# Kernel optimization log

Hardware: AMD Instinct MI355X
Metric: run time of the kernel (lower is better)

Reference implementation:

```python
import jax, jax.numpy as jnp
import numpy as np

# __init__ constants
COORS_RANGE = ((-51.2, 51.2), (-51.2, 51.2), (-4.0, 2.4))  # x, y, z ranges
SPATIAL = (512, 512, 64)  # base spatial shape (X, Y, Z)
SCALES = (2, 4, 8, 1)     # scale_list + [1]
N_POINTS = 2_000_000
N_BATCH = 8


def setup_inputs() -> dict:
    key = jax.random.key(0)
    kp, kb = jax.random.split(key)
    lo = jnp.array([r[0] for r in COORS_RANGE], dtype=jnp.float32)
    hi = jnp.array([r[1] for r in COORS_RANGE], dtype=jnp.float32)
    u = jax.random.uniform(kp, (N_POINTS, 3), dtype=jnp.float32)
    points = lo + u * (hi - lo)  # [N,3] xyz inside the voxelization range
    batch_idx = jax.random.randint(kb, (N_POINTS,), 0, N_BATCH).astype(jnp.int64)
    return {"points": points, "batch_idx": batch_idx}


def reference(points, batch_idx):
    """Per scale: quantize xyz to voxel indices, then unique/dedup with inverse and
    counts. Rows [b,x,y,z] are packed into a single int64 key so that a 1-D unique
    (lexicographically equivalent to torch.unique(dim=0)) can be used.
    Returns, for each scale in SCALES: (full_coors [N,4] int64, coors_inv [N] int,
    coors [M,4] int32 in [b,z,y,x] order), flattened into one tuple."""
    b = batch_idx.astype(jnp.int64)
    outs = []
    for scale in SCALES:
        dims = [int(np.ceil(s / scale)) for s in SPATIAL]  # per-scale grid size
        idxs = []
        for i in range(3):
            lo, hi = COORS_RANGE[i]
            # torch .long() truncates toward zero; values are >=0 in range so
            # truncation == floor here.
            idxs.append((dims[i] * (points[:, i] - lo) / (hi - lo)).astype(jnp.int64))
        xidx, yidx, zidx = idxs
        full_coors = jnp.stack([b, xidx, yidx, zidx], axis=-1)  # [N,4]
        sx, sy, sz = dims
        # pack (b,x,y,z) lexicographically into one key
        keys = ((b * sx + xidx) * sy + yidx) * sz + zidx
        unq, unq_inv, unq_cnt = jnp.unique(keys, return_inverse=True, return_counts=True)
        zb = unq % sz
        rem = unq // sz
        yb = rem % sy
        rem = rem // sy
        xb = rem % sx
        bb = rem // sx
        # original reorders unq columns to [b, z, y, x] and casts to int32
        coors = jnp.stack([bb, zb, yb, xb], axis=-1).astype(jnp.int32)
        outs.extend([full_coors, unq_inv.reshape(-1), coors])
    return tuple(outs)
```

## Files before the change

kernel.cpp:

```cpp
#include <hip/hip_runtime.h>
#include <stdint.h>


#define CHUNK 4096
#define NB    1174
#define TOTALW 4808704
#define R_S2 0
#define R_S4 528384
#define R_S8 598016
#define R_S1 610304
#define PAD0 524288
#define PAD1 593920
#define PAD2 606208
#define PAD3 4804608
#define NBUCKET 512
#define BCAP 5120
#define KEYBLOCKS 1024
#define ROUND 2048
#define KPT 8

__device__ __forceinline__ uint32_t cmp2(uint32_t w) {
  w = (w | (w >> 1)) & 0x55555555u;
  w = (w | (w >> 1)) & 0x33333333u;
  w = (w | (w >> 2)) & 0x0F0F0F0Fu;
  w = (w | (w >> 4)) & 0x00FF00FFu;
  w = (w | (w >> 8)) & 0x0000FFFFu;
  return w;
}

__global__ __launch_bounds__(256) void k_key(
    const float* __restrict__ pts, const int* __restrict__ bidx, int n,
    uint32_t* __restrict__ keys,
    uint32_t* __restrict__ bucketCount, uint32_t* __restrict__ bucketData) {
  __shared__ uint32_t cnt[NBUCKET], inc[NBUCKET], pos[NBUCKET], gpos[NBUCKET];
  __shared__ uint32_t shs[256];
  __shared__ uint32_t scratch[ROUND];
  int t = threadIdx.x;
  int base = blockIdx.x * ROUND;

  cnt[t] = 0; cnt[t + 256] = 0;
  pos[t] = 0; pos[t + 256] = 0;
  __syncthreads();

  uint32_t myKey[KPT];
  int myBk[KPT];
#pragma unroll
  for (int k = 0; k < KPT; k++) {
    int j = base + k * 256 + t;
    myBk[k] = -1;
    if (j < n) {
      float px = pts[3 * j + 0];
      float py = pts[3 * j + 1];
      float pz = pts[3 * j + 2];
      int b = bidx[j];
      int x1 = (int)((512.0f * (px + 51.2f)) / 102.4f);
      int y1 = (int)((512.0f * (py + 51.2f)) / 102.4f);
      int z1 = (int)((64.0f * (pz + 4.0f)) / 6.4f);
      keys[j] = ((uint32_t)b << 27) | ((uint32_t)x1 << 17) | ((uint32_t)y1 << 7) | (uint32_t)z1;
      uint32_t s1k = (uint32_t)(((b * 512 + x1) * 512 + y1) * 64 + z1);
      if (s1k < (1u << 27)) {
        int bk = (int)(s1k >> 18);
        myBk[k] = bk;
        myKey[k] = s1k;
        atomicAdd(&cnt[bk], 1u);
      }
    }
  }
  __syncthreads();

  uint32_t c0 = cnt[2 * t], c1 = cnt[2 * t + 1];
  gpos[2 * t] = c0 ? atomicAdd(&bucketCount[2 * t], c0) : 0u;
  gpos[2 * t + 1] = c1 ? atomicAdd(&bucketCount[2 * t + 1], c1) : 0u;
  uint32_t s = c0 + c1;
  shs[t] = s;
  __syncthreads();
  for (int off = 1; off < 256; off <<= 1) {
    uint32_t add = (t >= off) ? shs[t - off] : 0u;
    __syncthreads();
    shs[t] += add;
    __syncthreads();
  }
  inc[2 * t] = shs[t] - s + c0;
  inc[2 * t + 1] = shs[t];
  __syncthreads();
  uint32_t total = shs[255];

#pragma unroll
  for (int k = 0; k < KPT; k++) {
    if (myBk[k] >= 0) {
      int bk = myBk[k];
      uint32_t slot = inc[bk] - cnt[bk] + atomicAdd(&pos[bk], 1u);
      scratch[slot] = myKey[k];
    }
  }
  __syncthreads();

#pragma unroll
  for (int m = 0; m < KPT; m++) {
    uint32_t p = (uint32_t)(m * 256 + t);
    if (p < total) {
      uint32_t kk = scratch[p];
      int lo = (int)(kk >> 18);
      uint32_t lidx = p - (inc[lo] - cnt[lo]);
      uint32_t g = gpos[lo] + lidx;
      if (g < BCAP) bucketData[(size_t)lo * BCAP + g] = kk;
    }
  }
}

__device__ __forceinline__ uint32_t blockReduce(uint32_t v, uint32_t* shR, int t) {
  shR[t] = v;
  __syncthreads();
  for (int off = 128; off > 0; off >>= 1) {
    if (t < off) shR[t] += shR[t + off];
    __syncthreads();
  }
  uint32_t r = shR[0];
  __syncthreads();
  return r;
}

__global__ __launch_bounds__(256) void k_bucket(
    const uint32_t* __restrict__ bucketCount, const uint32_t* __restrict__ bucketData,
    uint32_t* __restrict__ bitmap, uint32_t* __restrict__ chunkSums) {
  __shared__ uint32_t s1L[8192];
  __shared__ uint32_t s2L[1024];
  __shared__ uint32_t s4L[128];
  __shared__ uint32_t shR[256];
  int bk = blockIdx.x, t = threadIdx.x;

  uint4 z4 = make_uint4(0, 0, 0, 0);
  for (int i = t; i < 2048; i += 256) ((uint4*)s1L)[i] = z4;

  if (bk < 4) {
    const int pads[4] = {PAD0, PAD1, PAD2, PAD3};
    uint4* pz = (uint4*)(bitmap + pads[bk]);
    for (int i = t; i < 1024; i += 256) pz[i] = z4;
  }
  __syncthreads();

  uint32_t c = bucketCount[bk];
  if (c > BCAP) c = BCAP;
  const uint32_t* src = bucketData + (size_t)bk * BCAP;
  for (uint32_t i = t; i < c; i += 256) {
    uint32_t key = src[i];
    uint32_t local = key & 0x3FFFFu;
    atomicOr(&s1L[local >> 5], 1u << (local & 31u));
  }
  __syncthreads();

  uint4* g1 = (uint4*)(bitmap + R_S1 + (size_t)bk * 8192);
  uint32_t pc1a = 0, pc1b = 0;
  for (int i = t; i < 2048; i += 256) {
    uint4 v = ((uint4*)s1L)[i];
    g1[i] = v;
    uint32_t pc = __popc(v.x) + __popc(v.y) + __popc(v.z) + __popc(v.w);
    if (i < 1024) pc1a += pc; else pc1b += pc;
  }

  for (int i = t; i < 1024; i += 256) {
    int x2r = i >> 8, Y2 = i & 255;
    int a = (2 * x2r * 512 + 2 * Y2) * 2;
    int b2 = ((2 * x2r + 1) * 512 + 2 * Y2) * 2;
    uint32_t Ax = s1L[a], Ay = s1L[a + 1], Az = s1L[a + 2], Aw = s1L[a + 3];
    uint32_t Bx = s1L[b2], By = s1L[b2 + 1], Bz = s1L[b2 + 2], Bw = s1L[b2 + 3];
    s2L[i] = cmp2(Ax | Az | Bx | Bz) | (cmp2(Ay | Aw | By | Bw) << 16);
  }
  __syncthreads();
  uint32_t pc2 = 0;
  for (int i = t; i < 1024; i += 256) {
    uint32_t v = s2L[i];
    bitmap[R_S2 + (size_t)bk * 1024 + i] = v;
    pc2 += __popc(v);
  }

  uint32_t pc4 = 0;
  if (t < 128) {
    int x4r = t >> 6, kk = t & 63;
    int a = (2 * x4r) * 256 + 4 * kk;
    int b4 = (2 * x4r + 1) * 256 + 4 * kk;
    uint32_t A0 = s2L[a], A1 = s2L[a + 1], A2 = s2L[a + 2], A3 = s2L[a + 3];
    uint32_t B0 = s2L[b4], B1 = s2L[b4 + 1], B2 = s2L[b4 + 2], B3 = s2L[b4 + 3];
    uint32_t v = cmp2(A0 | A1 | B0 | B1) | (cmp2(A2 | A3 | B2 | B3) << 16);
    s4L[t] = v;
    pc4 = __popc(v);
  }
  __syncthreads();
  if (t < 128) bitmap[R_S4 + (size_t)bk * 128 + t] = s4L[t];

  uint32_t pc8 = 0;
  if (t < 16) {
    uint32_t res = 0;
#pragma unroll
    for (int j = 0; j < 4; j++) {
      uint32_t u = s4L[4 * t + j] | s4L[64 + 4 * t + j];
      u = (u | (u >> 16)) & 0xFFFFu;
      res |= cmp2(u) << (8 * j);
    }
    bitmap[R_S8 + (size_t)bk * 16 + t] = res;
    pc8 = __popc(res);
  }

  uint32_t S1a = blockReduce(pc1a, shR, t);
  uint32_t S1b = blockReduce(pc1b, shR, t);
  uint32_t S2 = blockReduce(pc2, shR, t);
  uint32_t S4 = blockReduce(pc4, shR, t);
  uint32_t S8 = blockReduce(pc8, shR, t);
  if (t == 0) {
    chunkSums[149 + 2 * bk] = S1a;
    chunkSums[150 + 2 * bk] = S1b;
    atomicAdd(&chunkSums[bk >> 2], S2);
    atomicAdd(&chunkSums[129 + (bk >> 5)], S4);
    atomicAdd(&chunkSums[146 + (bk >> 8)], S8);
  }
}

__global__ __launch_bounds__(256) void k_scanB(
    uint32_t* blockSums, long long* devOff, uint32_t* devRank, long long fiveN) {
  __shared__ uint32_t sh[256];
  __shared__ uint32_t shB[3];
  int t = threadIdx.x;
  uint32_t v[8];
  uint32_t s = 0;
#pragma unroll
  for (int k = 0; k < 8; k++) {
    int idx = t * 8 + k;
    uint32_t x = (idx < NB) ? blockSums[idx] : 0u;
    v[k] = x;
    s += x;
  }
  sh[t] = s;
  __syncthreads();
  for (int off = 1; off < 256; off <<= 1) {
    uint32_t add = (t >= off) ? sh[t - off] : 0u;
    __syncthreads();
    sh[t] += add;
    __syncthreads();
  }
  uint32_t run = sh[t] - s;
#pragma unroll
  for (int k = 0; k < 8; k++) {
    int idx = t * 8 + k;
    if (idx < NB) blockSums[idx] = run;
    if (idx == 129) shB[0] = run;
    if (idx == 146) shB[1] = run;
    if (idx == 149) shB[2] = run;
    run += v[k];
  }
  __syncthreads();
  if (t == 0) {
    uint32_t tot = sh[255];
    uint32_t T0 = shB[0];
    uint32_t T1 = shB[1] - shB[0];
    uint32_t T2 = shB[2] - shB[1];
    uint32_t T3 = tot - shB[2];
    devOff[0] = 0;
    devOff[1] = devOff[0] + fiveN + 4LL * T0;
    devOff[2] = devOff[1] + fiveN + 4LL * T1;
    devOff[3] = devOff[2] + fiveN + 4LL * T2;
    devOff[4] = devOff[3] + fiveN + 4LL * T3;
    devRank[0] = 0;
    devRank[1] = shB[0];
    devRank[2] = shB[1];
    devRank[3] = shB[2];
  }
}

__global__ __launch_bounds__(256) void k_pref(
    const uint32_t* __restrict__ bitmap, const uint32_t* __restrict__ blockSums,
    uint2* __restrict__ pairs) {
  __shared__ uint32_t sh[256];
  int t = threadIdx.x;
  size_t w0 = (size_t)blockIdx.x * CHUNK + t * 16;
  const uint4* bp = (const uint4*)(bitmap + w0);
  uint4 words[4];
  uint32_t s = 0;
#pragma unroll
  for (int k = 0; k < 4; k++) {
    uint4 v = bp[k];
    words[k] = v;
    s += __popc(v.x) + __popc(v.y) + __popc(v.z) + __popc(v.w);
  }
  sh[t] = s;
  __syncthreads();
  for (int off = 1; off < 256; off <<= 1) {
    uint32_t add = (t >= off) ? sh[t - off] : 0u;
    __syncthreads();
    sh[t] += add;
    __syncthreads();
  }
  uint32_t run = blockSums[blockIdx.x] + (sh[t] - s);
  uint4* pp = (uint4*)(pairs + w0);
#pragma unroll
  for (int k = 0; k < 4; k++) {
    uint4 o1, o2;
    o1.x = words[k].x; o1.y = run; run += __popc(words[k].x);
    o1.z = words[k].y; o1.w = run; run += __popc(words[k].y);
    o2.x = words[k].z; o2.y = run; run += __popc(words[k].z);
    o2.z = words[k].w; o2.w = run; run += __popc(words[k].w);
    pp[2 * k] = o1;
    pp[2 * k + 1] = o2;
  }
}

__global__ __launch_bounds__(256) void k_write(
    const uint32_t* __restrict__ keys, int n, const uint2* __restrict__ pairs,
    const uint32_t* __restrict__ devRank, const long long* __restrict__ devOff,
    int* __restrict__ out, long long fourN) {
  const int SX[4] = {256, 128, 64, 512};
  const int SY[4] = {256, 128, 64, 512};
  const int SZ[4] = {32, 16, 8, 64};
  const int SH[4] = {1, 2, 3, 0};
  const int RG[4] = {R_S2, R_S4, R_S8, R_S1};
  long long off[4];
  uint32_t rnk[4];
#pragma unroll
  for (int i = 0; i < 4; i++) { off[i] = devOff[i]; rnk[i] = devRank[i]; }
#pragma unroll
  for (int half = 0; half < 2; half++) {
    int j = blockIdx.x * 512 + half * 256 + threadIdx.x;
    if (j >= n) continue;
    uint32_t p = keys[j];
    int b = (int)(p >> 27);
    int x1 = (int)((p >> 17) & 1023u);
    int y1 = (int)((p >> 7) & 1023u);
    int z1 = (int)(p & 127u);
#pragma unroll
    for (int i = 0; i < 4; i++) {
      int sh = SH[i];
      int xi = x1 >> sh, yi = y1 >> sh, zi = z1 >> sh;
      uint32_t key = (uint32_t)(((b * SX[i] + xi) * SY[i] + yi) * SZ[i] + zi);
      uint2 pr = pairs[RG[i] + (key >> 5)];
      long long o = off[i];
      *(int4*)(out + o + 4LL * j) = make_int4(b, xi, yi, zi);
      uint32_t inv = pr.y + __popc(pr.x & ((1u << (key & 31u)) - 1u)) - rnk[i];
      out[o + fourN + j] = (int)inv;
    }
  }
}

template <int LZ, int LYZ, int LB, int MZ, int MY, int MX, int RG, int SCALE_IDX>
__device__ __forceinline__ void uniq_region(
    uint32_t w, uint32_t wd, uint32_t pf, uint32_t rankBase,
    const long long* __restrict__ devOff, int* __restrict__ out, long long fiveN) {
  uint32_t pos = pf - rankBase;
  long long base = devOff[SCALE_IDX] + fiveN;
  uint32_t local = w - (uint32_t)RG;
  while (wd) {
    int bit = __ffs(wd) - 1;
    wd &= wd - 1u;
    uint32_t key = (local << 5) + (uint32_t)bit;
    int z = (int)(key & (uint32_t)MZ);
    int y = (int)((key >> LZ) & (uint32_t)MY);
    int x = (int)((key >> LYZ) & (uint32_t)MX);
    int bb = (int)(key >> LB);
    *(int4*)(out + base + 4LL * pos) = make_int4(bb, z, y, x);
    pos++;
  }
}

__global__ __launch_bounds__(256) void k_uniq(
    const uint2* __restrict__ pairs, const uint32_t* __restrict__ devRank,
    const long long* __restrict__ devOff, int* __restrict__ out, long long fiveN) {
  uint32_t w = blockIdx.x * 256 + threadIdx.x;
  uint2 pr = pairs[w];
  if (!pr.x) return;
  if (w < R_S4) {
    uniq_region<5, 13, 21, 31, 255, 255, R_S2, 0>(w, pr.x, pr.y, devRank[0], devOff, out, fiveN);
  } else if (w < R_S8) {
    uniq_region<4, 11, 18, 15, 127, 127, R_S4, 1>(w, pr.x, pr.y, devRank[1], devOff, out, fiveN);
  } else if (w < R_S1) {
    uniq_region<3, 9, 15, 7, 63, 63, R_S8, 2>(w, pr.x, pr.y, devRank[2], devOff, out, fiveN);
  } else {
    uniq_region<6, 15, 24, 63, 511, 511, R_S1, 3>(w, pr.x, pr.y, devRank[3], devOff, out, fiveN);
  }
}

extern "C" void kernel_launch(void* const* d_in, const int* in_sizes, int n_in,
                              void* d_out, int out_size, void* d_ws, size_t ws_size,
                              hipStream_t stream) {
  const float* pts = (const float*)d_in[0];
  const int* bidx = (const int*)d_in[1];
  int n = in_sizes[0] / 3;
  int* out = (int*)d_out;

  char* ws = (char*)d_ws;
  long long* devOff = (long long*)ws;
  uint32_t* devRank = (uint32_t*)(ws + 64);
  uint32_t* chunkSums = (uint32_t*)(ws + 256);
  uint32_t* bucketCount = (uint32_t*)(ws + 5120);
  uint32_t* bitmap = (uint32_t*)(ws + 8192);
  uint2* pairs = (uint2*)(ws + 19243008);
  uint32_t* keys = (uint32_t*)(ws + 57712640);
  uint32_t* bucketData = (uint32_t*)(ws + 65712640);

  const long long fourN = 4LL * n, fiveN = 5LL * n;
  const int gridW = (n + 511) / 512;

  hipMemsetAsync(chunkSums, 0, NB * 4, stream);
  hipMemsetAsync(bucketCount, 0, NBUCKET * 4, stream);
  hipLaunchKernelGGL(k_key, dim3(KEYBLOCKS), dim3(256), 0, stream,
                     pts, bidx, n, keys, bucketCount, bucketData);
  hipLaunchKernelGGL(k_bucket, dim3(NBUCKET), dim3(256), 0, stream,
                     bucketCount, bucketData, bitmap, chunkSums);
  hipLaunchKernelGGL(k_scanB, dim3(1), dim3(256), 0, stream, chunkSums, devOff, devRank, fiveN);
  hipLaunchKernelGGL(k_pref, dim3(NB), dim3(256), 0, stream, bitmap, chunkSums, pairs);
  hipLaunchKernelGGL(k_write, dim3(gridW), dim3(256), 0, stream,
                     keys, n, pairs, devRank, devOff, out, fourN);
  hipLaunchKernelGGL(k_uniq, dim3(TOTALW / 256), dim3(256), 0, stream,
                     pairs, devRank, devOff, out, fiveN);
}
```

Before: 449.4 us.

## Fuse write and unique kernels into one launch, split per scale, drop memset

Merges the per-point output kernel and the unique-coordinate kernel into a single launch. Blocks are partitioned so each block handles one scale for a slice of points, or a range of bitmap words. The chunkSums memset moves into block 0 of the key kernel. This removes two launches and lets the two output phases overlap, and giving each block a single scale should improve locality of the pairs lookups. The risk is that the chunkSums zeroing must finish before k_bucket reads it, which stream ordering guarantees here, and a hard-coded index range that depends on NB.

```diff
diff --git a/kernel.cpp b/kernel.cpp
--- a/kernel.cpp
+++ b/kernel.cpp
@@ -31,12 +31,18 @@
 __global__ __launch_bounds__(256) void k_key(
     const float* __restrict__ pts, const int* __restrict__ bidx, int n,
     uint32_t* __restrict__ keys,
-    uint32_t* __restrict__ bucketCount, uint32_t* __restrict__ bucketData) {
+    uint32_t* __restrict__ bucketCount, uint32_t* __restrict__ bucketData,
+    uint32_t* __restrict__ chunkSums) {
   __shared__ uint32_t cnt[NBUCKET], inc[NBUCKET], pos[NBUCKET], gpos[NBUCKET];
   __shared__ uint32_t shs[256];
   __shared__ uint32_t scratch[ROUND];
   int t = threadIdx.x;
   int base = blockIdx.x * ROUND;
+
+  if (blockIdx.x == 0) {
+    if (t < 149) chunkSums[t] = 0;
+    if (t == 149) chunkSums[1173] = 0;
+  }
 
   cnt[t] = 0; cnt[t + 256] = 0;
   pos[t] = 0; pos[t + 256] = 0;
@@ -303,42 +309,6 @@
   }
 }
 
-__global__ __launch_bounds__(256) void k_write(
-    const uint32_t* __restrict__ keys, int n, const uint2* __restrict__ pairs,
-    const uint32_t* __restrict__ devRank, const long long* __restrict__ devOff,
-    int* __restrict__ out, long long fourN) {
-  const int SX[4] = {256, 128, 64, 512};
-  const int SY[4] = {256, 128, 64, 512};
-  const int SZ[4] = {32, 16, 8, 64};
-  const int SH[4] = {1, 2, 3, 0};
-  const int RG[4] = {R_S2, R_S4, R_S8, R_S1};
-  long long off[4];
-  uint32_t rnk[4];
-#pragma unroll
-  for (int i = 0; i < 4; i++) { off[i] = devOff[i]; rnk[i] = devRank[i]; }
-#pragma unroll
-  for (int half = 0; half < 2; half++) {
-    int j = blockIdx.x * 512 + half * 256 + threadIdx.x;
-    if (j >= n) continue;
-    uint32_t p = keys[j];
-    int b = (int)(p >> 27);
-    int x1 = (int)((p >> 17) & 1023u);
-    int y1 = (int)((p >> 7) & 1023u);
-    int z1 = (int)(p & 127u);
-#pragma unroll
-    for (int i = 0; i < 4; i++) {
-      int sh = SH[i];
-      int xi = x1 >> sh, yi = y1 >> sh, zi = z1 >> sh;
-      uint32_t key = (uint32_t)(((b * SX[i] + xi) * SY[i] + yi) * SZ[i] + zi);
-      uint2 pr = pairs[RG[i] + (key >> 5)];
-      long long o = off[i];
-      *(int4*)(out + o + 4LL * j) = make_int4(b, xi, yi, zi);
-      uint32_t inv = pr.y + __popc(pr.x & ((1u << (key & 31u)) - 1u)) - rnk[i];
-      out[o + fourN + j] = (int)inv;
-    }
-  }
-}
-
 template <int LZ, int LYZ, int LB, int MZ, int MY, int MX, int RG, int SCALE_IDX>
 __device__ __forceinline__ void uniq_region(
     uint32_t w, uint32_t wd, uint32_t pf, uint32_t rankBase,
@@ -359,20 +329,53 @@
   }
 }
 
-__global__ __launch_bounds__(256) void k_uniq(
-    const uint2* __restrict__ pairs, const uint32_t* __restrict__ devRank,
-    const long long* __restrict__ devOff, int* __restrict__ out, long long fiveN) {
-  uint32_t w = blockIdx.x * 256 + threadIdx.x;
-  uint2 pr = pairs[w];
-  if (!pr.x) return;
-  if (w < R_S4) {
-    uniq_region<5, 13, 21, 31, 255, 255, R_S2, 0>(w, pr.x, pr.y, devRank[0], devOff, out, fiveN);
-  } else if (w < R_S8) {
-    uniq_region<4, 11, 18, 15, 127, 127, R_S4, 1>(w, pr.x, pr.y, devRank[1], devOff, out, fiveN);
-  } else if (w < R_S1) {
-    uniq_region<3, 9, 15, 7, 63, 63, R_S8, 2>(w, pr.x, pr.y, devRank[2], devOff, out, fiveN);
+__global__ __launch_bounds__(256) void k_out(
+    const uint32_t* __restrict__ keys, int n, const uint2* __restrict__ pairs,
+    const uint32_t* __restrict__ devRank, const long long* __restrict__ devOff,
+    int* __restrict__ out, long long fourN, long long fiveN, int NW) {
+  int bid = blockIdx.x;
+  int t = threadIdx.x;
+  if (bid < 4 * NW) {
+    int sec = bid / NW;
+    int wb = bid - sec * NW;
+    const int SCI[4] = {3, 0, 1, 2};
+    const int SX[4] = {256, 128, 64, 512};
+    const int SZ[4] = {32, 16, 8, 64};
+    const int SH[4] = {1, 2, 3, 0};
+    const int RG[4] = {R_S2, R_S4, R_S8, R_S1};
+    int i = SCI[sec];
+    int sh = SH[i], sx = SX[i], sz = SZ[i], rg = RG[i];
+    long long o = devOff[i];
+    uint32_t rnk = devRank[i];
+#pragma unroll
+    for (int half = 0; half < 2; half++) {
+      int j = wb * 512 + half * 256 + t;
+      if (j >= n) continue;
+      uint32_t p = keys[j];
+      int b = (int)(p >> 27);
+      int x1 = (int)((p >> 17) & 1023u);
+      int y1 = (int)((p >> 7) & 1023u);
+      int z1 = (int)(p & 127u);
+      int xi = x1 >> sh, yi = y1 >> sh, zi = z1 >> sh;
+      uint32_t key = (uint32_t)(((b * sx + xi) * sx + yi) * sz + zi);
+      uint2 pr = pairs[rg + (key >> 5)];
+      *(int4*)(out + o + 4LL * j) = make_int4(b, xi, yi, zi);
+      uint32_t inv = pr.y + __popc(pr.x & ((1u << (key & 31u)) - 1u)) - rnk;
+      out[o + fourN + j] = (int)inv;
+    }
   } else {
-    uniq_region<6, 15, 24, 63, 511, 511, R_S1, 3>(w, pr.x, pr.y, devRank[3], devOff, out, fiveN);
+    uint32_t w = (uint32_t)(bid - 4 * NW) * 256 + t;
+    uint2 pr = pairs[w];
+    if (!pr.x) return;
+    if (w < R_S4) {
+      uniq_region<5, 13, 21, 31, 255, 255, R_S2, 0>(w, pr.x, pr.y, devRank[0], devOff, out, fiveN);
+    } else if (w < R_S8) {
+      uniq_region<4, 11, 18, 15, 127, 127, R_S4, 1>(w, pr.x, pr.y, devRank[1], devOff, out, fiveN);
+    } else if (w < R_S1) {
+      uniq_region<3, 9, 15, 7, 63, 63, R_S8, 2>(w, pr.x, pr.y, devRank[2], devOff, out, fiveN);
+    } else {
+      uniq_region<6, 15, 24, 63, 511, 511, R_S1, 3>(w, pr.x, pr.y, devRank[3], devOff, out, fiveN);
+    }
   }
 }
 
@@ -395,18 +398,15 @@
   uint32_t* bucketData = (uint32_t*)(ws + 65712640);
 
   const long long fourN = 4LL * n, fiveN = 5LL * n;
-  const int gridW = (n + 511) / 512;
-
-  hipMemsetAsync(chunkSums, 0, NB * 4, stream);
+  const int NW = (n + 511) / 512;
+
   hipMemsetAsync(bucketCount, 0, NBUCKET * 4, stream);
   hipLaunchKernelGGL(k_key, dim3(KEYBLOCKS), dim3(256), 0, stream,
-                     pts, bidx, n, keys, bucketCount, bucketData);
+                     pts, bidx, n, keys, bucketCount, bucketData, chunkSums);
   hipLaunchKernelGGL(k_bucket, dim3(NBUCKET), dim3(256), 0, stream,
                      bucketCount, bucketData, bitmap, chunkSums);
   hipLaunchKernelGGL(k_scanB, dim3(1), dim3(256), 0, stream, chunkSums, devOff, devRank, fiveN);
   hipLaunchKernelGGL(k_pref, dim3(NB), dim3(256), 0, stream, bitmap, chunkSums, pairs);
-  hipLaunchKernelGGL(k_write, dim3(gridW), dim3(256), 0, stream,
-                     keys, n, pairs, devRank, devOff, out, fourN);
-  hipLaunchKernelGGL(k_uniq, dim3(TOTALW / 256), dim3(256), 0, stream,
-                     pairs, devRank, devOff, out, fiveN);
-}
+  hipLaunchKernelGGL(k_out, dim3(4 * NW + TOTALW / 256), dim3(256), 0, stream,
+                     keys, n, pairs, devRank, devOff, out, fourN, fiveN, NW);
+}
```

New measurement: 426.3 us. 1.05x faster.
